# Optimization experiments

Hardware: AMD Instinct MI355X
Metric: run time of the kernel (lower is better)

## Reference

```python
import jax, jax.numpy as jnp
import numpy as np

B = 65536

def setup_inputs() -> dict:
    key = jax.random.key(0)
    k1, k2 = jax.random.split(key, 2)
    x = jax.random.normal(k1, (B, 1, 28, 28), dtype=jnp.float32)
    # classifier params: Linear(4*14*14 -> 10)
    W = jax.random.normal(k2, (10, 4 * 14 * 14), dtype=jnp.float32) * 0.03
    b = jnp.zeros((10,), dtype=jnp.float32)
    return {"x": x, "W": W, "b": b}


def reference(x, W, b):
    # x: [B,1,28,28]
    batch = x.shape[0]
    img = x[:, 0]  # [B,28,28]
    # non-overlapping 2x2 patches, row-major over (r,c), flattened row-major
    # within patch -> matches torch's x[:, r:r+2, c:c+2].view(B, -1)
    patches = img.reshape(batch, 14, 2, 14, 2).transpose(0, 1, 3, 2, 4)
    patches = patches.reshape(batch, 196, 4)
    # Exact closed form of the 4-qubit circuit RY(theta_i) on wire i followed
    # by CNOT chain (0->1->2->3) and <Z_k> measurement:
    #   <Z_k> = prod_{j<=k} cos(theta_j)
    ez = jnp.cumprod(jnp.cos(patches), axis=-1)  # [B,196,4]
    feat = ez.reshape(batch, 4 * 14 * 14)  # [B,784]
    logits = feat @ W.T + b  # [B,10]
    return jax.nn.log_softmax(logits, axis=-1)
```

## Files before the change

kernel.cpp:

```cpp
#include <hip/hip_runtime.h>

#define NCLS 10
#define NUM_IMG 65536

__device__ __forceinline__ void async_cp16(const float* g, float* l) {
    __builtin_amdgcn_global_load_lds(
        (const __attribute__((address_space(1))) void*)(g),
        (__attribute__((address_space(3))) void*)(l),
        16, 0, 0);
}

__global__ __launch_bounds__(448, 4) void quanv_logits_kernel(
    const float* __restrict__ x,
    const float* __restrict__ W,
    const float* __restrict__ bias,
    float* __restrict__ out)
{
    __shared__ float4 sb[2][896];
    __shared__ float  sW[7840];

    const int tid  = threadIdx.x;
    const int w    = __builtin_amdgcn_readfirstlane(tid >> 6);
    const int lane = tid & 63;
    const int img0 = blockIdx.x << 6;

    {
        const float4* Wg = reinterpret_cast<const float4*>(W);
        float4* Wl = reinterpret_cast<float4*>(sW);
#pragma unroll
        for (int r = 0; r < 5; ++r) {
            const int idx = tid + r * 448;
            if (idx < 1960) Wl[idx] = Wg[idx];
        }
    }

    const int s0 = tid, s1 = tid + 448;
    const float* g0 = x + (size_t)(img0 + s0 / 14) * 784 + (s0 % 14) * 4;
    const float* g1 = x + (size_t)(img0 + s1 / 14) * 784 + (s1 % 14) * 4;

    float acc[NCLS];
#pragma unroll
    for (int c = 0; c < NCLS; ++c) acc[c] = 0.0f;

    async_cp16(g0, (float*)&sb[0][s0]);
    async_cp16(g1, (float*)&sb[0][s1]);
    __syncthreads();

#pragma unroll
    for (int rr = 0; rr < 14; ++rr) {
        const int cur = rr & 1, nxt = cur ^ 1;
        if (rr < 13) {
            async_cp16(g0 + (rr + 1) * 56, (float*)&sb[nxt][s0]);
            async_cp16(g1 + (rr + 1) * 56, (float*)&sb[nxt][s1]);
        }

        const float4 t4 = sb[cur][lane * 14 + w];
        const float4 b4 = sb[cur][lane * 14 + w + 7];

        const float e0 = __cosf(t4.x);
        const float e1 = e0 * __cosf(t4.y);
        const float e2 = e1 * __cosf(b4.x);
        const float e3 = e2 * __cosf(b4.y);
        const float f0 = __cosf(t4.z);
        const float f1 = f0 * __cosf(t4.w);
        const float f2 = f1 * __cosf(b4.z);
        const float f3 = f2 * __cosf(b4.w);

        const int P = (rr * 14 + 2 * w) * 4;
#pragma unroll
        for (int c = 0; c < NCLS; ++c) {
            const float4 wa = *reinterpret_cast<const float4*>(&sW[c * 784 + P]);
            const float4 wb = *reinterpret_cast<const float4*>(&sW[c * 784 + P + 4]);
            float a = acc[c];
            a = fmaf(e0, wa.x, a); a = fmaf(e1, wa.y, a);
            a = fmaf(e2, wa.z, a); a = fmaf(e3, wa.w, a);
            a = fmaf(f0, wb.x, a); a = fmaf(f1, wb.y, a);
            a = fmaf(f2, wb.z, a); a = fmaf(f3, wb.w, a);
            acc[c] = a;
        }
        __syncthreads();
    }

    float* part = (float*)sb;
#pragma unroll
    for (int c = 0; c < NCLS; ++c) part[lane * 71 + w * NCLS + c] = acc[c];
    __syncthreads();

    if (w == 0) {
        float s[NCLS];
#pragma unroll
        for (int c = 0; c < NCLS; ++c) s[c] = bias[c];
        for (int ww = 0; ww < 7; ++ww) {
#pragma unroll
            for (int c = 0; c < NCLS; ++c) s[c] += part[lane * 71 + ww * NCLS + c];
        }
        float m = s[0];
#pragma unroll
        for (int c = 1; c < NCLS; ++c) m = fmaxf(m, s[c]);
        float sum = 0.0f;
#pragma unroll
        for (int c = 0; c < NCLS; ++c) sum += __expf(s[c] - m);
        const float lse = __logf(sum) + m;

        float* o = out + (size_t)(img0 + lane) * NCLS;
#pragma unroll
        for (int c = 0; c < NCLS; c += 2) {
            float2 v;
            v.x = s[c]     - lse;
            v.y = s[c + 1] - lse;
            *reinterpret_cast<float2*>(o + c) = v;
        }
    }
}

extern "C" void kernel_launch(void* const* d_in, const int* in_sizes, int n_in,
                              void* d_out, int out_size, void* d_ws, size_t ws_size,
                              hipStream_t stream) {
    const float* x    = (const float*)d_in[0];
    const float* W    = (const float*)d_in[1];
    const float* bias = (const float*)d_in[2];
    float* out        = (float*)d_out;

    dim3 block(448);
    dim3 grid(NUM_IMG / 64);
    quanv_logits_kernel<<<grid, block, 0, stream>>>(x, W, bias, out);
}
```

Measured before the change: 291.0 us.

## Process two images per thread with direct global loads, dropping LDS staging

Each block now handles 128 images instead of 64. Each thread computes two images, so every weight read from LDS is reused for both. The async global-to-LDS double-buffered staging of x and the per-row __syncthreads are removed, and threads read their float4 patches straight from global memory. This cuts LDS weight traffic and barrier overhead, but the direct loads are strided by 784 floats across lanes, so they are poorly coalesced. Register pressure also rises under the 448x4 launch bounds.

New measurement: 317.1 us. 1.09x slower.

```diff
diff --git a/kernel.cpp b/kernel.cpp
--- a/kernel.cpp
+++ b/kernel.cpp
@@ -2,13 +2,6 @@
 
 #define NCLS 10
 #define NUM_IMG 65536
-
-__device__ __forceinline__ void async_cp16(const float* g, float* l) {
-    __builtin_amdgcn_global_load_lds(
-        (const __attribute__((address_space(1))) void*)(g),
-        (__attribute__((address_space(3))) void*)(l),
-        16, 0, 0);
-}
 
 __global__ __launch_bounds__(448, 4) void quanv_logits_kernel(
     const float* __restrict__ x,
@@ -16,13 +9,13 @@
     const float* __restrict__ bias,
     float* __restrict__ out)
 {
-    __shared__ float4 sb[2][896];
-    __shared__ float  sW[7840];
+    __shared__ float sW[7840];
+    __shared__ float part[128 * 71];
 
     const int tid  = threadIdx.x;
     const int w    = __builtin_amdgcn_readfirstlane(tid >> 6);
     const int lane = tid & 63;
-    const int img0 = blockIdx.x << 6;
+    const int img0 = blockIdx.x << 7;
 
     {
         const float4* Wg = reinterpret_cast<const float4*>(W);
@@ -34,65 +27,76 @@
         }
     }
 
-    const int s0 = tid, s1 = tid + 448;
-    const float* g0 = x + (size_t)(img0 + s0 / 14) * 784 + (s0 % 14) * 4;
-    const float* g1 = x + (size_t)(img0 + s1 / 14) * 784 + (s1 % 14) * 4;
+    const float* pA = x + (size_t)(img0 + lane) * 784;
+    const float* pB = x + (size_t)(img0 + 64 + lane) * 784;
 
-    float acc[NCLS];
+    float accA[NCLS], accB[NCLS];
 #pragma unroll
-    for (int c = 0; c < NCLS; ++c) acc[c] = 0.0f;
+    for (int c = 0; c < NCLS; ++c) { accA[c] = 0.0f; accB[c] = 0.0f; }
 
-    async_cp16(g0, (float*)&sb[0][s0]);
-    async_cp16(g1, (float*)&sb[0][s1]);
     __syncthreads();
 
 #pragma unroll
     for (int rr = 0; rr < 14; ++rr) {
-        const int cur = rr & 1, nxt = cur ^ 1;
-        if (rr < 13) {
-            async_cp16(g0 + (rr + 1) * 56, (float*)&sb[nxt][s0]);
-            async_cp16(g1 + (rr + 1) * 56, (float*)&sb[nxt][s1]);
-        }
+        const int offT = rr * 56 + w * 4;
+        const int offB = rr * 56 + (w + 7) * 4;
+        const float4 tA = *reinterpret_cast<const float4*>(pA + offT);
+        const float4 bA = *reinterpret_cast<const float4*>(pA + offB);
+        const float4 tB = *reinterpret_cast<const float4*>(pB + offT);
+        const float4 bB = *reinterpret_cast<const float4*>(pB + offB);
 
-        const float4 t4 = sb[cur][lane * 14 + w];
-        const float4 b4 = sb[cur][lane * 14 + w + 7];
-
-        const float e0 = __cosf(t4.x);
-        const float e1 = e0 * __cosf(t4.y);
-        const float e2 = e1 * __cosf(b4.x);
-        const float e3 = e2 * __cosf(b4.y);
-        const float f0 = __cosf(t4.z);
-        const float f1 = f0 * __cosf(t4.w);
-        const float f2 = f1 * __cosf(b4.z);
-        const float f3 = f2 * __cosf(b4.w);
+        const float eA0 = __cosf(tA.x);
+        const float eA1 = eA0 * __cosf(tA.y);
+        const float eA2 = eA1 * __cosf(bA.x);
+        const float eA3 = eA2 * __cosf(bA.y);
+        const float fA0 = __cosf(tA.z);
+        const float fA1 = fA0 * __cosf(tA.w);
+        const float fA2 = fA1 * __cosf(bA.z);
+        const float fA3 = fA2 * __cosf(bA.w);
+        const float eB0 = __cosf(tB.x);
+        const float eB1 = eB0 * __cosf(tB.y);
+        const float eB2 = eB1 * __cosf(bB.x);
+        const float eB3 = eB2 * __cosf(bB.y);
+        const float fB0 = __cosf(tB.z);
+        const float fB1 = fB0 * __cosf(tB.w);
+        const float fB2 = fB1 * __cosf(bB.z);
+        const float fB3 = fB2 * __cosf(bB.w);
 
         const int P = (rr * 14 + 2 * w) * 4;
 #pragma unroll
         for (int c = 0; c < NCLS; ++c) {
             const float4 wa = *reinterpret_cast<const float4*>(&sW[c * 784 + P]);
             const float4 wb = *reinterpret_cast<const float4*>(&sW[c * 784 + P + 4]);
-            float a = acc[c];
-            a = fmaf(e0, wa.x, a); a = fmaf(e1, wa.y, a);
-            a = fmaf(e2, wa.z, a); a = fmaf(e3, wa.w, a);
-            a = fmaf(f0, wb.x, a); a = fmaf(f1, wb.y, a);
-            a = fmaf(f2, wb.z, a); a = fmaf(f3, wb.w, a);
-            acc[c] = a;
+            float a = accA[c];
+            a = fmaf(eA0, wa.x, a); a = fmaf(eA1, wa.y, a);
+            a = fmaf(eA2, wa.z, a); a = fmaf(eA3, wa.w, a);
+            a = fmaf(fA0, wb.x, a); a = fmaf(fA1, wb.y, a);
+            a = fmaf(fA2, wb.z, a); a = fmaf(fA3, wb.w, a);
+            accA[c] = a;
+            float b2 = accB[c];
+            b2 = fmaf(eB0, wa.x, b2); b2 = fmaf(eB1, wa.y, b2);
+            b2 = fmaf(eB2, wa.z, b2); b2 = fmaf(eB3, wa.w, b2);
+            b2 = fmaf(fB0, wb.x, b2); b2 = fmaf(fB1, wb.y, b2);
+            b2 = fmaf(fB2, wb.z, b2); b2 = fmaf(fB3, wb.w, b2);
+            accB[c] = b2;
         }
-        __syncthreads();
     }
 
-    float* part = (float*)sb;
 #pragma unroll
-    for (int c = 0; c < NCLS; ++c) part[lane * 71 + w * NCLS + c] = acc[c];
+    for (int c = 0; c < NCLS; ++c) {
+        part[lane * 71 + w * NCLS + c]         = accA[c];
+        part[(64 + lane) * 71 + w * NCLS + c]  = accB[c];
+    }
     __syncthreads();
 
-    if (w == 0) {
+    if (w < 2) {
+        const int iL = (w << 6) + lane;
         float s[NCLS];
 #pragma unroll
         for (int c = 0; c < NCLS; ++c) s[c] = bias[c];
         for (int ww = 0; ww < 7; ++ww) {
 #pragma unroll
-            for (int c = 0; c < NCLS; ++c) s[c] += part[lane * 71 + ww * NCLS + c];
+            for (int c = 0; c < NCLS; ++c) s[c] += part[iL * 71 + ww * NCLS + c];
         }
         float m = s[0];
 #pragma unroll
@@ -102,7 +106,7 @@
         for (int c = 0; c < NCLS; ++c) sum += __expf(s[c] - m);
         const float lse = __logf(sum) + m;
 
-        float* o = out + (size_t)(img0 + lane) * NCLS;
+        float* o = out + (size_t)(img0 + iL) * NCLS;
 #pragma unroll
         for (int c = 0; c < NCLS; c += 2) {
             float2 v;
@@ -122,6 +126,6 @@
     float* out        = (float*)d_out;
 
     dim3 block(448);
-    dim3 grid(NUM_IMG / 64);
+    dim3 grid(NUM_IMG / 128);
     quanv_logits_kernel<<<grid, block, 0, stream>>>(x, W, bias, out);
 }
```
